# Kernel tuning notes

Hardware: AMD Instinct MI355X
Metric: run time of the kernel (lower is better)

Reference implementation:

```python
import jax, jax.numpy as jnp
import numpy as np

N_PROTS = 2048
MOLS_PER_PROT = 8
N_MOLS = N_PROTS * MOLS_PER_PROT
DIM = 768
MARGIN = 0.5


def setup_inputs() -> dict:
    key = jax.random.key(0)
    k1, k2, k3 = jax.random.split(key, 3)
    prot_emb = jax.random.normal(k1, (N_PROTS, DIM), dtype=jnp.float32)
    mol_emb = jax.random.normal(k2, (N_MOLS, DIM), dtype=jnp.float32)
    # L2-normalize like typical CLIP-style retrieval embeddings
    prot_emb = prot_emb / jnp.linalg.norm(prot_emb, axis=1, keepdims=True)
    mol_emb = mol_emb / jnp.linalg.norm(mol_emb, axis=1, keepdims=True)
    # block-structured labels: protein i paired with mols [8i, 8i+8)
    rows = jnp.repeat(jnp.arange(N_PROTS), MOLS_PER_PROT)
    cols = jnp.arange(N_MOLS)
    labels = jnp.zeros((N_PROTS, N_MOLS), dtype=jnp.float32).at[rows, cols].set(1.0)
    # pIC50 values in [2, 10]
    pic50_matrix = 2.0 + 8.0 * jax.random.uniform(k3, (N_PROTS, N_MOLS), dtype=jnp.float32)
    logit_scale = jnp.float32(1.0 / 0.07)
    return {"prot_emb": prot_emb, "mol_emb": mol_emb, "labels": labels,
            "pic50_matrix": pic50_matrix, "logit_scale": logit_scale}


def reference(prot_emb, mol_emb, labels, pic50_matrix, logit_scale):
    n_prots = prot_emb.shape[0]
    n_mols = mol_emb.shape[0]
    sim = jnp.matmul(prot_emb, mol_emb.T) * logit_scale  # [n_prots, n_mols]

    # affinity-weighted InfoNCE (prot -> mol)
    pic50_norm = jnp.clip((pic50_matrix - 2.0) / 8.0, 0.0, 1.0)
    pos_w = labels * pic50_norm
    pos_w = pos_w / (pos_w.sum(axis=1, keepdims=True) + 1e-8)
    loss_p2m = -jnp.sum(pos_w * jax.nn.log_softmax(sim, axis=1)) / n_prots

    # mol -> prot NLL
    mol_labels = jnp.argmax(labels, axis=0)  # [n_mols]
    lsm_m2p = jax.nn.log_softmax(sim.T, axis=1)  # [n_mols, n_prots]
    loss_m2p = -jnp.mean(lsm_m2p[jnp.arange(n_mols), mol_labels])

    # pairwise margin-ranking among positives (exactly MOLS_PER_PROT positives per protein)
    P = MOLS_PER_PROT
    _, pos_idx = jax.lax.top_k(labels, P)  # [n_prots, P] indices of positives
    pos_pic = jnp.take_along_axis(pic50_matrix, pos_idx, axis=1)  # [n_prots, P]
    pos_sc = jnp.take_along_axis(sim, pos_idx, axis=1)            # [n_prots, P]
    dp = pos_pic[:, :, None] - pos_pic[:, None, :]  # [n_prots, P, P]
    ds = pos_sc[:, :, None] - pos_sc[:, None, :]
    pair = jnp.where(dp > 0, jax.nn.relu(MARGIN - ds),
                     jnp.where(dp < 0, jax.nn.relu(MARGIN + ds), 0.0))
    upper = jnp.triu(jnp.ones((P, P), dtype=bool), k=1)  # unordered pairs j<k
    n_pairs = n_prots * (P * (P - 1) // 2)
    ranking_loss = jnp.sum(jnp.where(upper[None], pair, 0.0)) / n_pairs

    # negative push-down
    neg_loss = jnp.mean(jax.nn.relu(sim * (1.0 - labels)))

    total = loss_p2m + loss_m2p + 0.5 * ranking_loss + 0.1 * neg_loss
    return (total, loss_p2m, loss_m2p, ranking_loss, neg_loss)
```

## Files before the change

kernel.cpp:

```cpp
#include <hip/hip_runtime.h>
#include <hip/hip_bf16.h>
#include <math.h>

#define N_PROTS 2048
#define N_MOLS  16384
#define DIM     768
#define SHIFT   16.0f
#define MARGIN  0.5f

typedef __attribute__((ext_vector_type(8))) short short8;
typedef __attribute__((ext_vector_type(4))) float f32x4;
typedef __attribute__((ext_vector_type(4))) unsigned short us4;
typedef __attribute__((ext_vector_type(8))) unsigned short us8;

__device__ __forceinline__ unsigned short bf16rnd(float x) {
    unsigned int u = __float_as_uint(x);
    u += 0x7fffu + ((u >> 16) & 1u);
    return (unsigned short)(u >> 16);
}

__device__ __forceinline__ void gload16(const void* g, void* l) {
    __builtin_amdgcn_global_load_lds(
        (const __attribute__((address_space(1))) unsigned int*)g,
        (__attribute__((address_space(3))) unsigned int*)l, 16, 0, 0);
}

#define ACC_FLOATS 34824
#define PROT_BF_OFF_B 139296ull
#define PROT_BF_BYTES (2048ull*768*2)
#define MOL_BF_OFF_B  (PROT_BF_OFF_B + PROT_BF_BYTES)
#define MOL_BF_BYTES  (16384ull*768*2)
#define WS_NEED       (MOL_BF_OFF_B + MOL_BF_BYTES)

__global__ __launch_bounds__(256)
void convert_bf16(const float* __restrict__ prot, const float* __restrict__ mol,
                  unsigned short* __restrict__ protBf, unsigned short* __restrict__ molBf)
{
    const size_t PROT_G = (size_t)N_PROTS * DIM / 8;
    size_t t = (size_t)blockIdx.x * 256 + threadIdx.x;
    const float* src;
    unsigned short* dst;
    if (t < PROT_G) { src = prot + t * 8; dst = protBf + t * 8; }
    else            { size_t u = t - PROT_G; src = mol + u * 8; dst = molBf + u * 8; }
    float4 v0 = ((const float4*)src)[0];
    float4 v1 = ((const float4*)src)[1];
    us8 o;
    o[0] = bf16rnd(v0.x); o[1] = bf16rnd(v0.y); o[2] = bf16rnd(v0.z); o[3] = bf16rnd(v0.w);
    o[4] = bf16rnd(v1.x); o[5] = bf16rnd(v1.y); o[6] = bf16rnd(v1.z); o[7] = bf16rnd(v1.w);
    *(us8*)dst = o;
}

__global__ __launch_bounds__(512, 2)
void sim_pass_bf16_v2(const unsigned short* __restrict__ protBf,
                      const unsigned short* __restrict__ molBf,
                      const float* __restrict__ scale_p,
                      float* __restrict__ row_se, float* __restrict__ col_se,
                      float* __restrict__ pos_sim, float* __restrict__ scalars)
{
    __shared__ unsigned short As[4][256][32];
    __shared__ unsigned short Bs[4][256][32];
    __shared__ float redBuf[8];

    const int tid = threadIdx.x;
    const int bid  = blockIdx.x;
    const int xcd  = bid & 7;
    const int sl8  = bid >> 3;
    const int bx   = xcd * 8 + (sl8 & 7);
    const int by   = sl8 >> 3;
    const int rowBase = by * 256;
    const int colBase = bx * 256;

    const int wave = tid >> 6;
    const int lane = tid & 63;
    const int wm = wave >> 2;
    const int wn = wave & 3;
    const int l15 = lane & 15;
    const int q   = lane >> 4;

    const int rsub = lane >> 2;
    const int cs   = lane & 3;
    const int swz  = (cs ^ (rsub & 3)) << 3;
    const unsigned short* aP =
        protBf + (size_t)(rowBase + wave * 32 + rsub) * DIM + swz;
    const unsigned short* bP =
        molBf  + (size_t)(colBase + wave * 32 + rsub) * DIM + swz;

#define STAGE_A(sl, kt) do { \
    gload16(aP + (size_t)(kt) * 32,                    &As[sl][wave * 32][0]);      \
    gload16(aP + (size_t)(kt) * 32 + (size_t)16 * DIM, &As[sl][wave * 32 + 16][0]); \
} while (0)
#define STAGE_B(sl, kt) do { \
    gload16(bP + (size_t)(kt) * 32,                    &Bs[sl][wave * 32][0]);      \
    gload16(bP + (size_t)(kt) * 32 + (size_t)16 * DIM, &Bs[sl][wave * 32 + 16][0]); \
} while (0)

    f32x4 acc[8][4];
#pragma unroll
    for (int i = 0; i < 8; ++i)
#pragma unroll
        for (int j = 0; j < 4; ++j) acc[i][j] = (f32x4){0.f, 0.f, 0.f, 0.f};

    STAGE_A(0, 0); STAGE_B(0, 0);
    STAGE_A(1, 1); STAGE_B(1, 1);
    STAGE_A(2, 2); STAGE_B(2, 2);

    const int fArow = wm * 128 + l15;
    const int fBrow = wn * 64 + l15;
    const int fsw   = (q ^ (l15 & 3)) << 3;

#pragma unroll 1
    for (int t = 0; t < 24; ++t) {
        const int sl   = t & 3;
        const int pf   = (t + 3) & 3;
        const int kpre = (t < 21) ? (t + 3) : (t - 5);
        asm volatile("s_waitcnt vmcnt(8)" ::: "memory");
        __builtin_amdgcn_s_barrier();

        short8 aF[4], bF[4];
#pragma unroll
        for (int ni = 0; ni < 4; ++ni)
            bF[ni] = *(const short8*)&Bs[sl][fBrow + ni * 16][fsw];
#pragma unroll
        for (int mi = 0; mi < 4; ++mi)
            aF[mi] = *(const short8*)&As[sl][fArow + mi * 16][fsw];
        STAGE_A(pf, kpre);
        __builtin_amdgcn_s_setprio(1);
#pragma unroll
        for (int mi = 0; mi < 4; ++mi)
#pragma unroll
            for (int ni = 0; ni < 4; ++ni)
                acc[mi][ni] = __builtin_amdgcn_mfma_f32_16x16x32_bf16(
                    aF[mi], bF[ni], acc[mi][ni], 0, 0, 0);
        __builtin_amdgcn_s_setprio(0);

#pragma unroll
        for (int mi = 0; mi < 4; ++mi)
            aF[mi] = *(const short8*)&As[sl][fArow + 64 + mi * 16][fsw];
        STAGE_B(pf, kpre);
        __builtin_amdgcn_s_setprio(1);
#pragma unroll
        for (int mi = 0; mi < 4; ++mi)
#pragma unroll
            for (int ni = 0; ni < 4; ++ni)
                acc[4 + mi][ni] = __builtin_amdgcn_mfma_f32_16x16x32_bf16(
                    aF[mi], bF[ni], acc[4 + mi][ni], 0, 0, 0);
        __builtin_amdgcn_s_setprio(0);
    }
#undef STAGE_A
#undef STAGE_B

    const float scale = scale_p[0];
    float csum[4] = {0.f, 0.f, 0.f, 0.f};
    float rl = 0.f;
#pragma unroll
    for (int mi = 0; mi < 8; ++mi) {
        float rs[4] = {0.f, 0.f, 0.f, 0.f};
#pragma unroll
        for (int ni = 0; ni < 4; ++ni) {
#pragma unroll
            for (int r = 0; r < 4; ++r) {
                float sim = acc[mi][ni][r] * scale;
                float e = __expf(sim - SHIFT);
                rs[r] += e;
                csum[ni] += e;
                rl += fmaxf(sim, 0.f);
                int rg = rowBase + wm * 128 + mi * 16 + q * 4 + r;
                int cg = colBase + wn * 64 + ni * 16 + l15;
                if ((cg >> 3) == rg) pos_sim[cg] = sim;
            }
        }
#pragma unroll
        for (int r = 0; r < 4; ++r) {
            float v = rs[r];
            v += __shfl_xor(v, 1); v += __shfl_xor(v, 2);
            v += __shfl_xor(v, 4); v += __shfl_xor(v, 8);
            if (l15 == 0)
                atomicAdd(&row_se[rowBase + wm * 128 + mi * 16 + q * 4 + r], v);
        }
    }
#pragma unroll
    for (int ni = 0; ni < 4; ++ni) {
        float v = csum[ni];
        v += __shfl_xor(v, 16); v += __shfl_xor(v, 32);
        if (q == 0)
            atomicAdd(&col_se[colBase + wn * 64 + ni * 16 + l15], v);
    }
#pragma unroll
    for (int m = 1; m < 64; m <<= 1) rl += __shfl_xor(rl, m);
    if (lane == 0) redBuf[wave] = rl;
    __syncthreads();
    if (tid == 0) {
        float s = 0.f;
#pragma unroll
        for (int w = 0; w < 8; ++w) s += redBuf[w];
        atomicAdd(&scalars[0], s);
    }
}

__global__ __launch_bounds__(256, 2)
void sim_pass(const float* __restrict__ prot, const float* __restrict__ mol,
              const float* __restrict__ scale_p,
              float* __restrict__ row_se, float* __restrict__ col_se,
              float* __restrict__ pos_sim, float* __restrict__ scalars)
{
    __shared__ unsigned short As[128][32];
    __shared__ unsigned short Bs[128][32];
    __shared__ float redBuf[4];

    const int tid = threadIdx.x;
    const int rowBase = blockIdx.y * 128;
    const int colBase = blockIdx.x * 128;
    const int wave = tid >> 6;
    const int lane = tid & 63;
    const int wr = (wave >> 1) * 64;
    const int wc = (wave & 1) * 64;
    const int l15 = lane & 15;
    const int q   = lane >> 4;

    f32x4 acc[4][4];
#pragma unroll
    for (int i = 0; i < 4; ++i)
#pragma unroll
        for (int j = 0; j < 4; ++j) acc[i][j] = (f32x4){0.f, 0.f, 0.f, 0.f};

    const float* aBase = prot + (size_t)rowBase * DIM;
    const float* bBase = mol  + (size_t)colBase * DIM;
    float4 aReg[4], bReg[4];
#pragma unroll
    for (int i = 0; i < 4; ++i) {
        int f = tid + 256 * i;
        int row = f >> 3, c4 = f & 7;
        aReg[i] = *(const float4*)(aBase + (size_t)row * DIM + (c4 << 2));
        bReg[i] = *(const float4*)(bBase + (size_t)row * DIM + (c4 << 2));
    }
#pragma unroll 1
    for (int s = 0; s < DIM / 32; ++s) {
#pragma unroll
        for (int i = 0; i < 4; ++i) {
            int f = tid + 256 * i;
            int row = f >> 3, c4 = f & 7;
            us4 av, bv;
            av.x = bf16rnd(aReg[i].x); av.y = bf16rnd(aReg[i].y);
            av.z = bf16rnd(aReg[i].z); av.w = bf16rnd(aReg[i].w);
            bv.x = bf16rnd(bReg[i].x); bv.y = bf16rnd(bReg[i].y);
            bv.z = bf16rnd(bReg[i].z); bv.w = bf16rnd(bReg[i].w);
            *(us4*)&As[row][c4 << 2] = av;
            *(us4*)&Bs[row][c4 << 2] = bv;
        }
        __syncthreads();
        if (s + 1 < DIM / 32) {
            int k0 = (s + 1) * 32;
#pragma unroll
            for (int i = 0; i < 4; ++i) {
                int f = tid + 256 * i;
                int row = f >> 3, c4 = f & 7;
                aReg[i] = *(const float4*)(aBase + (size_t)row * DIM + k0 + (c4 << 2));
                bReg[i] = *(const float4*)(bBase + (size_t)row * DIM + k0 + (c4 << 2));
            }
        }
        short8 aF[4], bF[4];
#pragma unroll
        for (int mi = 0; mi < 4; ++mi) aF[mi] = *(const short8*)&As[wr + mi * 16 + l15][q * 8];
#pragma unroll
        for (int ni = 0; ni < 4; ++ni) bF[ni] = *(const short8*)&Bs[wc + ni * 16 + l15][q * 8];
#pragma unroll
        for (int mi = 0; mi < 4; ++mi)
#pragma unroll
            for (int ni = 0; ni < 4; ++ni)
                acc[mi][ni] = __builtin_amdgcn_mfma_f32_16x16x32_bf16(aF[mi], bF[ni], acc[mi][ni], 0, 0, 0);
        __syncthreads();
    }

    const float scale = scale_p[0];
    float rsum[4][4];
    float csum[4] = {0.f, 0.f, 0.f, 0.f};
    float rl = 0.f;
#pragma unroll
    for (int mi = 0; mi < 4; ++mi)
#pragma unroll
        for (int r = 0; r < 4; ++r) rsum[mi][r] = 0.f;
#pragma unroll
    for (int mi = 0; mi < 4; ++mi) {
#pragma unroll
        for (int ni = 0; ni < 4; ++ni) {
#pragma unroll
            for (int r = 0; r < 4; ++r) {
                float sim = acc[mi][ni][r] * scale;
                float e = __expf(sim - SHIFT);
                rsum[mi][r] += e;
                csum[ni] += e;
                rl += fmaxf(sim, 0.f);
                int rg = rowBase + wr + mi * 16 + q * 4 + r;
                int cg = colBase + wc + ni * 16 + l15;
                if ((cg >> 3) == rg) pos_sim[cg] = sim;
            }
        }
    }
#pragma unroll
    for (int mi = 0; mi < 4; ++mi) {
#pragma unroll
        for (int r = 0; r < 4; ++r) {
            float v = rsum[mi][r];
            v += __shfl_xor(v, 1); v += __shfl_xor(v, 2);
            v += __shfl_xor(v, 4); v += __shfl_xor(v, 8);
            if (l15 == 0)
                atomicAdd(&row_se[rowBase + wr + mi * 16 + q * 4 + r], v);
        }
    }
#pragma unroll
    for (int ni = 0; ni < 4; ++ni) {
        float v = csum[ni];
        v += __shfl_xor(v, 16); v += __shfl_xor(v, 32);
        if (q == 0)
            atomicAdd(&col_se[colBase + wc + ni * 16 + l15], v);
    }
#pragma unroll
    for (int m = 1; m < 64; m <<= 1) rl += __shfl_xor(rl, m);
    if (lane == 0) redBuf[wave] = rl;
    __syncthreads();
    if (tid == 0)
        atomicAdd(&scalars[0], redBuf[0] + redBuf[1] + redBuf[2] + redBuf[3]);
}

__global__ __launch_bounds__(256)
void finalize1(const float* __restrict__ row_se, const float* __restrict__ col_se,
               const float* __restrict__ pos_sim, const float* __restrict__ pic50,
               float* __restrict__ scalars)
{
    int j = blockIdx.x * 256 + threadIdx.x;
    float m2p = SHIFT + __logf(col_se[j]) - pos_sim[j];

    float p2m = 0.f, rank = 0.f, prelu = 0.f;
    if ((j & 7) == 0) {
        int i = j >> 3;
        float s[8], pc[8], pr[8];
#pragma unroll
        for (int p = 0; p < 8; ++p) {
            s[p]  = pos_sim[j + p];
            pr[p] = pic50[(size_t)i * N_MOLS + j + p];
            float x = (pr[p] - 2.0f) * 0.125f;
            pc[p] = fminf(fmaxf(x, 0.f), 1.f);
            prelu += fmaxf(s[p], 0.f);
        }
        float wsum = 1e-8f;
#pragma unroll
        for (int p = 0; p < 8; ++p) wsum += pc[p];
        float lse = SHIFT + __logf(row_se[i]);
        float accp = 0.f;
#pragma unroll
        for (int p = 0; p < 8; ++p) accp += pc[p] * (lse - s[p]);
        p2m = accp / wsum;
#pragma unroll
        for (int a = 0; a < 8; ++a)
#pragma unroll
            for (int b = a + 1; b < 8; ++b) {
                float dp = pr[a] - pr[b];
                float ds = s[a] - s[b];
                float v = (dp > 0.f) ? fmaxf(MARGIN - ds, 0.f)
                        : ((dp < 0.f) ? fmaxf(MARGIN + ds, 0.f) : 0.f);
                rank += v;
            }
    }

#pragma unroll
    for (int m = 1; m < 64; m <<= 1) {
        m2p   += __shfl_xor(m2p, m);
        p2m   += __shfl_xor(p2m, m);
        rank  += __shfl_xor(rank, m);
        prelu += __shfl_xor(prelu, m);
    }
    __shared__ float rbuf[4][4];
    int wave = threadIdx.x >> 6, lane = threadIdx.x & 63;
    if (lane == 0) { rbuf[wave][0] = m2p; rbuf[wave][1] = p2m; rbuf[wave][2] = rank; rbuf[wave][3] = prelu; }
    __syncthreads();
    if (threadIdx.x == 0) {
        float a = 0, b = 0, c = 0, d = 0;
        for (int w = 0; w < 4; ++w) { a += rbuf[w][0]; b += rbuf[w][1]; c += rbuf[w][2]; d += rbuf[w][3]; }
        atomicAdd(&scalars[2], a);
        atomicAdd(&scalars[1], b);
        atomicAdd(&scalars[3], c);
        atomicAdd(&scalars[4], d);
    }
}

__global__ void finalize2(const float* __restrict__ scalars, float* __restrict__ out)
{
    float relu_neg = scalars[0] - scalars[4];
    float p2m  = scalars[1] / (float)N_PROTS;
    float m2p  = scalars[2] / (float)N_MOLS;
    float rank = scalars[3] / ((float)N_PROTS * 28.0f);
    float neg  = relu_neg / ((float)N_PROTS * (float)N_MOLS);
    out[0] = p2m + m2p + 0.5f * rank + 0.1f * neg;
    out[1] = p2m;
    out[2] = m2p;
    out[3] = rank;
    out[4] = neg;
}

extern "C" void kernel_launch(void* const* d_in, const int* in_sizes, int n_in,
                              void* d_out, int out_size, void* d_ws, size_t ws_size,
                              hipStream_t stream) {
    const float* prot   = (const float*)d_in[0];
    const float* mol    = (const float*)d_in[1];
    const float* pic50  = (const float*)d_in[3];
    const float* lscale = (const float*)d_in[4];

    float* ws      = (float*)d_ws;
    float* row_se  = ws;
    float* col_se  = ws + 2048;
    float* pos_sim = ws + 2048 + 16384;
    float* scalars = ws + 2048 + 16384 + 16384;

    hipMemsetAsync(d_ws, 0, (size_t)ACC_FLOATS * sizeof(float), stream);

    if (ws_size >= WS_NEED) {
        unsigned short* protBf = (unsigned short*)((char*)d_ws + PROT_BF_OFF_B);
        unsigned short* molBf  = (unsigned short*)((char*)d_ws + MOL_BF_OFF_B);
        size_t groups = ((size_t)N_PROTS + N_MOLS) * DIM / 8;
        convert_bf16<<<(unsigned)(groups / 256), 256, 0, stream>>>(prot, mol, protBf, molBf);
        sim_pass_bf16_v2<<<512, 512, 0, stream>>>(protBf, molBf, lscale, row_se, col_se, pos_sim, scalars);
    } else {
        dim3 grid(N_MOLS / 128, N_PROTS / 128);
        sim_pass<<<grid, 256, 0, stream>>>(prot, mol, lscale, row_se, col_se, pos_sim, scalars);
    }
    finalize1<<<N_MOLS / 256, 256, 0, stream>>>(row_se, col_se, pos_sim, pic50, scalars);
    finalize2<<<1, 1, 0, stream>>>(scalars, (float*)d_out);
}
```

Baseline: 381.1 us.

## Process two row tiles per block, fuse memset and finalize kernels

The similarity GEMM grid is halved to 256 blocks, and each block now computes two 256-row tiles that share the same column tile. The prefetch pipeline runs continuously across the tile boundary, which keeps col-sum partials in registers and cuts column atomics in half. The workspace memset is folded into the bf16 conversion kernel, and the two finalize kernels are merged into a single one-block kernel, which removes launches. The LDS swizzle function is also changed. In exchange, the 256-block grid may underfill the 256 CUs at two blocks per CU, and the single-block finalize serializes the reduction work.

```diff
diff --git a/kernel.cpp b/kernel.cpp
--- a/kernel.cpp
+++ b/kernel.cpp
@@ -24,6 +24,8 @@
         (const __attribute__((address_space(1))) unsigned int*)g,
         (__attribute__((address_space(3))) unsigned int*)l, 16, 0, 0);
 }
+
+__device__ __forceinline__ int sig4(int x) { return (x + (x >> 2)) & 3; }
 
 #define ACC_FLOATS 34824
 #define PROT_BF_OFF_B 139296ull
@@ -34,10 +36,15 @@
 
 __global__ __launch_bounds__(256)
 void convert_bf16(const float* __restrict__ prot, const float* __restrict__ mol,
-                  unsigned short* __restrict__ protBf, unsigned short* __restrict__ molBf)
+                  unsigned short* __restrict__ protBf, unsigned short* __restrict__ molBf,
+                  float* __restrict__ wsZero)
 {
     const size_t PROT_G = (size_t)N_PROTS * DIM / 8;
     size_t t = (size_t)blockIdx.x * 256 + threadIdx.x;
+    if (t < ACC_FLOATS / 4) {
+        float4 z = {0.f, 0.f, 0.f, 0.f};
+        ((float4*)wsZero)[t] = z;
+    }
     const float* src;
     unsigned short* dst;
     if (t < PROT_G) { src = prot + t * 8; dst = protBf + t * 8; }
@@ -51,7 +58,7 @@
 }
 
 __global__ __launch_bounds__(512, 2)
-void sim_pass_bf16_v2(const unsigned short* __restrict__ protBf,
+void sim_pass_bf16_v3(const unsigned short* __restrict__ protBf,
                       const unsigned short* __restrict__ molBf,
                       const float* __restrict__ scale_p,
                       float* __restrict__ row_se, float* __restrict__ col_se,
@@ -62,13 +69,13 @@
     __shared__ float redBuf[8];
 
     const int tid = threadIdx.x;
-    const int bid  = blockIdx.x;
-    const int xcd  = bid & 7;
-    const int sl8  = bid >> 3;
-    const int bx   = xcd * 8 + (sl8 & 7);
-    const int by   = sl8 >> 3;
-    const int rowBase = by * 256;
-    const int colBase = bx * 256;
+    const int bid = blockIdx.x;
+    const int xcd = bid & 7;
+    const int s8  = bid >> 3;
+    const int bx  = xcd * 8 + (s8 & 7);
+    const int byp = s8 >> 3;
+    const int rowBase0 = byp * 256;
+    const int colBase  = bx * 256;
 
     const int wave = tid >> 6;
     const int lane = tid & 63;
@@ -79,19 +86,20 @@
 
     const int rsub = lane >> 2;
     const int cs   = lane & 3;
-    const int swz  = (cs ^ (rsub & 3)) << 3;
+    const int csrc = (cs ^ sig4(rsub)) << 3;
     const unsigned short* aP =
-        protBf + (size_t)(rowBase + wave * 32 + rsub) * DIM + swz;
+        protBf + (size_t)(rowBase0 + wave * 32 + rsub) * DIM + csrc;
     const unsigned short* bP =
-        molBf  + (size_t)(colBase + wave * 32 + rsub) * DIM + swz;
-
-#define STAGE_A(sl, kt) do { \
-    gload16(aP + (size_t)(kt) * 32,                    &As[sl][wave * 32][0]);      \
-    gload16(aP + (size_t)(kt) * 32 + (size_t)16 * DIM, &As[sl][wave * 32 + 16][0]); \
+        molBf  + (size_t)(colBase  + wave * 32 + rsub) * DIM + csrc;
+    const size_t A_CT = (size_t)1024 * DIM;
+
+#define STAGE_A(sl, ptr) do { \
+    gload16((ptr),                     &As[sl][wave * 32][0]);      \
+    gload16((ptr) + (size_t)16 * DIM,  &As[sl][wave * 32 + 16][0]); \
 } while (0)
-#define STAGE_B(sl, kt) do { \
-    gload16(bP + (size_t)(kt) * 32,                    &Bs[sl][wave * 32][0]);      \
-    gload16(bP + (size_t)(kt) * 32 + (size_t)16 * DIM, &Bs[sl][wave * 32 + 16][0]); \
+#define STAGE_B(sl, ptr) do { \
+    gload16((ptr),                     &Bs[sl][wave * 32][0]);      \
+    gload16((ptr) + (size_t)16 * DIM,  &Bs[sl][wave * 32 + 16][0]); \
 } while (0)
 
     f32x4 acc[8][4];
@@ -100,84 +108,114 @@
 #pragma unroll
         for (int j = 0; j < 4; ++j) acc[i][j] = (f32x4){0.f, 0.f, 0.f, 0.f};
 
-    STAGE_A(0, 0); STAGE_B(0, 0);
-    STAGE_A(1, 1); STAGE_B(1, 1);
-    STAGE_A(2, 2); STAGE_B(2, 2);
+    STAGE_A(0, aP);      STAGE_B(0, bP);
+    STAGE_A(1, aP + 32); STAGE_B(1, bP + 32);
+    STAGE_A(2, aP + 64); STAGE_B(2, bP + 64);
 
     const int fArow = wm * 128 + l15;
     const int fBrow = wn * 64 + l15;
-    const int fsw   = (q ^ (l15 & 3)) << 3;
-
-#pragma unroll 1
-    for (int t = 0; t < 24; ++t) {
-        const int sl   = t & 3;
-        const int pf   = (t + 3) & 3;
-        const int kpre = (t < 21) ? (t + 3) : (t - 5);
-        asm volatile("s_waitcnt vmcnt(8)" ::: "memory");
-        __builtin_amdgcn_s_barrier();
-
-        short8 aF[4], bF[4];
-#pragma unroll
-        for (int ni = 0; ni < 4; ++ni)
-            bF[ni] = *(const short8*)&Bs[sl][fBrow + ni * 16][fsw];
-#pragma unroll
-        for (int mi = 0; mi < 4; ++mi)
-            aF[mi] = *(const short8*)&As[sl][fArow + mi * 16][fsw];
-        STAGE_A(pf, kpre);
-        __builtin_amdgcn_s_setprio(1);
-#pragma unroll
-        for (int mi = 0; mi < 4; ++mi)
-#pragma unroll
-            for (int ni = 0; ni < 4; ++ni)
-                acc[mi][ni] = __builtin_amdgcn_mfma_f32_16x16x32_bf16(
-                    aF[mi], bF[ni], acc[mi][ni], 0, 0, 0);
-        __builtin_amdgcn_s_setprio(0);
-
-#pragma unroll
-        for (int mi = 0; mi < 4; ++mi)
-            aF[mi] = *(const short8*)&As[sl][fArow + 64 + mi * 16][fsw];
-        STAGE_B(pf, kpre);
-        __builtin_amdgcn_s_setprio(1);
-#pragma unroll
-        for (int mi = 0; mi < 4; ++mi)
-#pragma unroll
-            for (int ni = 0; ni < 4; ++ni)
-                acc[4 + mi][ni] = __builtin_amdgcn_mfma_f32_16x16x32_bf16(
-                    aF[mi], bF[ni], acc[4 + mi][ni], 0, 0, 0);
-        __builtin_amdgcn_s_setprio(0);
-    }
-#undef STAGE_A
-#undef STAGE_B
+    const int fsw   = (q ^ sig4(l15)) << 3;
 
     const float scale = scale_p[0];
     float csum[4] = {0.f, 0.f, 0.f, 0.f};
     float rl = 0.f;
-#pragma unroll
-    for (int mi = 0; mi < 8; ++mi) {
-        float rs[4] = {0.f, 0.f, 0.f, 0.f};
-#pragma unroll
-        for (int ni = 0; ni < 4; ++ni) {
-#pragma unroll
-            for (int r = 0; r < 4; ++r) {
-                float sim = acc[mi][ni][r] * scale;
-                float e = __expf(sim - SHIFT);
-                rs[r] += e;
-                csum[ni] += e;
-                rl += fmaxf(sim, 0.f);
-                int rg = rowBase + wm * 128 + mi * 16 + q * 4 + r;
-                int cg = colBase + wn * 64 + ni * 16 + l15;
-                if ((cg >> 3) == rg) pos_sim[cg] = sim;
-            }
-        }
-#pragma unroll
-        for (int r = 0; r < 4; ++r) {
-            float v = rs[r];
-            v += __shfl_xor(v, 1); v += __shfl_xor(v, 2);
-            v += __shfl_xor(v, 4); v += __shfl_xor(v, 8);
-            if (l15 == 0)
-                atomicAdd(&row_se[rowBase + wm * 128 + mi * 16 + q * 4 + r], v);
-        }
-    }
+
+#define TILE_BODY(sl, pf, aPt, bPt) do {                                      \
+    asm volatile("s_waitcnt vmcnt(8)" ::: "memory");                          \
+    __builtin_amdgcn_s_barrier();                                             \
+    short8 aF[4], bF[4];                                                      \
+    _Pragma("unroll")                                                         \
+    for (int ni = 0; ni < 4; ++ni)                                            \
+        bF[ni] = *(const short8*)&Bs[sl][fBrow + ni * 16][fsw];               \
+    _Pragma("unroll")                                                         \
+    for (int mi = 0; mi < 4; ++mi)                                            \
+        aF[mi] = *(const short8*)&As[sl][fArow + mi * 16][fsw];               \
+    STAGE_A(pf, aPt);                                                         \
+    __builtin_amdgcn_s_setprio(1);                                            \
+    _Pragma("unroll")                                                         \
+    for (int mi = 0; mi < 4; ++mi)                                            \
+        _Pragma("unroll")                                                     \
+        for (int ni = 0; ni < 4; ++ni)                                        \
+            acc[mi][ni] = __builtin_amdgcn_mfma_f32_16x16x32_bf16(            \
+                aF[mi], bF[ni], acc[mi][ni], 0, 0, 0);                        \
+    __builtin_amdgcn_s_setprio(0);                                            \
+    _Pragma("unroll")                                                         \
+    for (int mi = 0; mi < 4; ++mi)                                            \
+        aF[mi] = *(const short8*)&As[sl][fArow + 64 + mi * 16][fsw];          \
+    STAGE_B(pf, bPt);                                                         \
+    __builtin_amdgcn_s_setprio(1);                                            \
+    _Pragma("unroll")                                                         \
+    for (int mi = 0; mi < 4; ++mi)                                            \
+        _Pragma("unroll")                                                     \
+        for (int ni = 0; ni < 4; ++ni)                                        \
+            acc[4 + mi][ni] = __builtin_amdgcn_mfma_f32_16x16x32_bf16(        \
+                aF[mi], bF[ni], acc[4 + mi][ni], 0, 0, 0);                    \
+    __builtin_amdgcn_s_setprio(0);                                            \
+} while (0)
+
+#define EPILOG(rowBaseX) do {                                                 \
+    _Pragma("unroll")                                                         \
+    for (int mi = 0; mi < 8; ++mi) {                                          \
+        float rs[4] = {0.f, 0.f, 0.f, 0.f};                                   \
+        _Pragma("unroll")                                                     \
+        for (int ni = 0; ni < 4; ++ni) {                                      \
+            _Pragma("unroll")                                                 \
+            for (int r = 0; r < 4; ++r) {                                     \
+                float sim = acc[mi][ni][r] * scale;                           \
+                float e = __expf(sim - SHIFT);                                \
+                rs[r] += e;                                                   \
+                csum[ni] += e;                                                \
+                rl += fmaxf(sim, 0.f);                                        \
+                int rg = (rowBaseX) + wm * 128 + mi * 16 + q * 4 + r;         \
+                int cg = colBase + wn * 64 + ni * 16 + l15;                   \
+                if ((cg >> 3) == rg) pos_sim[cg] = sim;                       \
+            }                                                                 \
+        }                                                                     \
+        _Pragma("unroll")                                                     \
+        for (int r = 0; r < 4; ++r) {                                         \
+            float v = rs[r];                                                  \
+            v += __shfl_xor(v, 1); v += __shfl_xor(v, 2);                     \
+            v += __shfl_xor(v, 4); v += __shfl_xor(v, 8);                     \
+            if (l15 == 0)                                                     \
+                atomicAdd(&row_se[(rowBaseX) + wm * 128 + mi * 16 + q * 4 + r], v); \
+        }                                                                     \
+    }                                                                         \
+} while (0)
+
+#pragma unroll 1
+    for (int t = 0; t < 24; ++t) {
+        const int u   = t + 3;
+        const int ctU = (u >= 24);
+        const int ktU = u - (ctU ? 24 : 0);
+        const unsigned short* aPt = aP + (ctU ? A_CT : 0) + (size_t)ktU * 32;
+        const unsigned short* bPt = bP + (size_t)ktU * 32;
+        TILE_BODY(t & 3, u & 3, aPt, bPt);
+    }
+
+    EPILOG(rowBase0);
+#pragma unroll
+    for (int i = 0; i < 8; ++i)
+#pragma unroll
+        for (int j = 0; j < 4; ++j) acc[i][j] = (f32x4){0.f, 0.f, 0.f, 0.f};
+
+#pragma unroll 1
+    for (int t = 24; t < 48; ++t) {
+        const int u  = t + 3;
+        const int uu = (u < 48) ? u : (u - 8);
+        const int ktU = uu - 24;
+        const unsigned short* aPt = aP + A_CT + (size_t)ktU * 32;
+        const unsigned short* bPt = bP + (size_t)ktU * 32;
+        TILE_BODY(t & 3, u & 3, aPt, bPt);
+    }
+    asm volatile("s_waitcnt vmcnt(0)" ::: "memory");
+
+    EPILOG(rowBase0 + 1024);
+
+#undef STAGE_A
+#undef STAGE_B
+#undef TILE_BODY
+#undef EPILOG
+
 #pragma unroll
     for (int ni = 0; ni < 4; ++ni) {
         float v = csum[ni];
@@ -190,10 +228,10 @@
     if (lane == 0) redBuf[wave] = rl;
     __syncthreads();
     if (tid == 0) {
-        float s = 0.f;
-#pragma unroll
-        for (int w = 0; w < 8; ++w) s += redBuf[w];
-        atomicAdd(&scalars[0], s);
+        float sv = 0.f;
+#pragma unroll
+        for (int w = 0; w < 8; ++w) sv += redBuf[w];
+        atomicAdd(&scalars[0], sv);
     }
 }
 
@@ -323,21 +361,23 @@
 }
 
 __global__ __launch_bounds__(256)
-void finalize1(const float* __restrict__ row_se, const float* __restrict__ col_se,
-               const float* __restrict__ pos_sim, const float* __restrict__ pic50,
-               float* __restrict__ scalars)
+void finalize_all(const float* __restrict__ row_se, const float* __restrict__ col_se,
+                  const float* __restrict__ pos_sim, const float* __restrict__ pic50,
+                  const float* __restrict__ scalars, float* __restrict__ out)
 {
-    int j = blockIdx.x * 256 + threadIdx.x;
-    float m2p = SHIFT + __logf(col_se[j]) - pos_sim[j];
-
-    float p2m = 0.f, rank = 0.f, prelu = 0.f;
-    if ((j & 7) == 0) {
-        int i = j >> 3;
+    const int tid = threadIdx.x;
+    float m2p = 0.f, p2m = 0.f, rank = 0.f, prelu = 0.f;
+
+    for (int j = tid; j < N_MOLS; j += 256)
+        m2p += SHIFT + __logf(col_se[j]) - pos_sim[j];
+
+    for (int i = tid; i < N_PROTS; i += 256) {
+        const int j0 = i << 3;
         float s[8], pc[8], pr[8];
 #pragma unroll
         for (int p = 0; p < 8; ++p) {
-            s[p]  = pos_sim[j + p];
-            pr[p] = pic50[(size_t)i * N_MOLS + j + p];
+            s[p]  = pos_sim[j0 + p];
+            pr[p] = pic50[(size_t)i * N_MOLS + j0 + p];
             float x = (pr[p] - 2.0f) * 0.125f;
             pc[p] = fminf(fmaxf(x, 0.f), 1.f);
             prelu += fmaxf(s[p], 0.f);
@@ -349,7 +389,7 @@
         float accp = 0.f;
 #pragma unroll
         for (int p = 0; p < 8; ++p) accp += pc[p] * (lse - s[p]);
-        p2m = accp / wsum;
+        p2m += accp / wsum;
 #pragma unroll
         for (int a = 0; a < 8; ++a)
 #pragma unroll
@@ -370,31 +410,25 @@
         prelu += __shfl_xor(prelu, m);
     }
     __shared__ float rbuf[4][4];
-    int wave = threadIdx.x >> 6, lane = threadIdx.x & 63;
-    if (lane == 0) { rbuf[wave][0] = m2p; rbuf[wave][1] = p2m; rbuf[wave][2] = rank; rbuf[wave][3] = prelu; }
+    const int wave = tid >> 6, lane = tid & 63;
+    if (lane == 0) { rbuf[wave][0] = m2p; rbuf[wave][1] = p2m;
+                     rbuf[wave][2] = rank; rbuf[wave][3] = prelu; }
     __syncthreads();
-    if (threadIdx.x == 0) {
+    if (tid == 0) {
         float a = 0, b = 0, c = 0, d = 0;
-        for (int w = 0; w < 4; ++w) { a += rbuf[w][0]; b += rbuf[w][1]; c += rbuf[w][2]; d += rbuf[w][3]; }
-        atomicAdd(&scalars[2], a);
-        atomicAdd(&scalars[1], b);
-        atomicAdd(&scalars[3], c);
-        atomicAdd(&scalars[4], d);
-    }
-}
-
-__global__ void finalize2(const float* __restrict__ scalars, float* __restrict__ out)
-{
-    float relu_neg = scalars[0] - scalars[4];
-    float p2m  = scalars[1] / (float)N_PROTS;
-    float m2p  = scalars[2] / (float)N_MOLS;
-    float rank = scalars[3] / ((float)N_PROTS * 28.0f);
-    float neg  = relu_neg / ((float)N_PROTS * (float)N_MOLS);
-    out[0] = p2m + m2p + 0.5f * rank + 0.1f * neg;
-    out[1] = p2m;
-    out[2] = m2p;
-    out[3] = rank;
-    out[4] = neg;
+        for (int w = 0; w < 4; ++w) { a += rbuf[w][0]; b += rbuf[w][1];
+                                      c += rbuf[w][2]; d += rbuf[w][3]; }
+        float relu_neg = scalars[0] - d;
+        float p2mv  = b / (float)N_PROTS;
+        float m2pv  = a / (float)N_MOLS;
+        float rankv = c / ((float)N_PROTS * 28.0f);
+        float negv  = relu_neg / ((float)N_PROTS * (float)N_MOLS);
+        out[0] = p2mv + m2pv + 0.5f * rankv + 0.1f * negv;
+        out[1] = p2mv;
+        out[2] = m2pv;
+        out[3] = rankv;
+        out[4] = negv;
+    }
 }
 
 extern "C" void kernel_launch(void* const* d_in, const int* in_sizes, int n_in,
@@ -411,18 +445,16 @@
     float* pos_sim = ws + 2048 + 16384;
     float* scalars = ws + 2048 + 16384 + 16384;
 
-    hipMemsetAsync(d_ws, 0, (size_t)ACC_FLOATS * sizeof(float), stream);
-
     if (ws_size >= WS_NEED) {
         unsigned short* protBf = (unsigned short*)((char*)d_ws + PROT_BF_OFF_B);
         unsigned short* molBf  = (unsigned short*)((char*)d_ws + MOL_BF_OFF_B);
         size_t groups = ((size_t)N_PROTS + N_MOLS) * DIM / 8;
-        convert_bf16<<<(unsigned)(groups / 256), 256, 0, stream>>>(prot, mol, protBf, molBf);
-        sim_pass_bf16_v2<<<512, 512, 0, stream>>>(protBf, molBf, lscale, row_se, col_se, pos_sim, scalars);
+        convert_bf16<<<(unsigned)(groups / 256), 256, 0, stream>>>(prot, mol, protBf, molBf, ws);
+        sim_pass_bf16_v3<<<256, 512, 0, stream>>>(protBf, molBf, lscale, row_se, col_se, pos_sim, scalars);
     } else {
+        hipMemsetAsync(d_ws, 0, (size_t)ACC_FLOATS * sizeof(float), stream);
         dim3 grid(N_MOLS / 128, N_PROTS / 128);
         sim_pass<<<grid, 256, 0, stream>>>(prot, mol, lscale, row_se, col_se, pos_sim, scalars);
     }
-    finalize1<<<N_MOLS / 256, 256, 0, stream>>>(row_se, col_se, pos_sim, pic50, scalars);
-    finalize2<<<1, 1, 0, stream>>>(scalars, (float*)d_out);
-}
+    finalize_all<<<1, 256, 0, stream>>>(row_se, col_se, pos_sim, pic50, scalars, (float*)d_out);
+}
```

Measured after the change: 507.9 us. 33.3% more time.
